# Kernel tuning notes

Measured on AMD Instinct MI355X. Metric: run time of the kernel, lower is better.

The kernel has to match this reference:

```python
import jax, jax.numpy as jnp
import numpy as np

B, N, QD, H, D = 2, 2048, 1152, 16, 72
INNER = H * D
RETAIN_RATE = 0.4  # layer_count in [4, 64] branch
N_KEEP = int(N * RETAIN_RATE)
N_PRUNE = N - N_KEEP
SCALE = D ** (-0.5)


def setup_inputs() -> dict:
    key = jax.random.key(0)
    ks = jax.random.split(key, 6)
    s = 0.02
    return {
        "x": jax.random.normal(ks[0], (B, N, QD), jnp.float32),
        "Wq": jax.random.normal(ks[1], (QD, INNER), jnp.float32) * s,
        "Wk": jax.random.normal(ks[2], (QD, INNER), jnp.float32) * s,
        "Wv": jax.random.normal(ks[3], (QD, INNER), jnp.float32) * s,
        "Wo": jax.random.normal(ks[4], (INNER, QD), jnp.float32) * s,
        "bo": jnp.zeros((QD,), jnp.float32),
    }


def reference(x, Wq, Wk, Wv, Wo, bo):
    b = x.shape[0]
    # self-attention: context = x
    q = (x @ Wq).reshape(b, N, H, D).transpose(0, 2, 1, 3)  # [b,H,N,D]
    k = (x @ Wk).reshape(b, N, H, D).transpose(0, 2, 1, 3)
    v = (x @ Wv).reshape(b, N, H, D).transpose(0, 2, 1, 3)

    # ---- WPR pruning pass: full attention map, mean over heads ----
    logits = jnp.einsum('bhnd,bhmd->bhnm', q, k) * SCALE  # [b,H,N,N]
    M = jax.nn.softmax(logits, axis=-1)
    attn = M.mean(axis=1)  # [b,N,N]

    # 5-step power iteration: dist = (1/N) @ attn^5
    dist = jnp.full((b, 1, N), 1.0 / N, dtype=attn.dtype)
    for _ in range(5):
        dist = dist @ attn
    importance = dist[:, 0]  # [b,N]

    _, imp_inds = jax.lax.top_k(importance, N_KEEP)
    _, prune_inds = jax.lax.top_k(-importance, N_PRUNE)
    # boolean-mask selection in torch returns rows in ascending index order
    sorted_imp = jnp.sort(imp_inds, axis=1)      # [b,N_KEEP]
    sorted_prune = jnp.sort(prune_inds, axis=1)  # [b,N_PRUNE]

    selected_rows = jnp.take_along_axis(attn, sorted_imp[:, :, None], axis=1)  # [b,N_KEEP,N]
    max_inds = jnp.argmax(selected_rows, axis=1)  # [b,N]: most-attending retained row per token
    sim_inds = jnp.take_along_axis(max_inds, sorted_prune, axis=1)  # [b,N_PRUNE]

    # ---- attention among retained tokens only ----
    gi = sorted_imp[:, None, :, None]  # broadcast gather index
    q_r = jnp.take_along_axis(q, gi, axis=2)  # [b,H,N_KEEP,D]
    k_r = jnp.take_along_axis(k, gi, axis=2)
    v_r = jnp.take_along_axis(v, gi, axis=2)
    attn_r = jax.nn.softmax(jnp.einsum('bhnd,bhmd->bhnm', q_r, k_r) * SCALE, axis=-1)
    out_r = jnp.einsum('bhnm,bhmd->bhnd', attn_r, v_r)  # [b,H,N_KEEP,D]
    out_r = out_r.transpose(0, 2, 1, 3).reshape(b, N_KEEP, INNER)

    # similarity-based recovery for pruned tokens
    out_p = jnp.take_along_axis(out_r, sim_inds[:, :, None], axis=1)  # [b,N_PRUNE,INNER]

    bidx = jnp.arange(b)[:, None]
    out = jnp.zeros((b, N, INNER), out_r.dtype)
    out = out.at[bidx, sorted_imp].set(out_r)
    out = out.at[bidx, sorted_prune].set(out_p)

    return out @ Wo + bo
```

## Files before the change

### kernel.cpp

```cpp
#include <hip/hip_runtime.h>

namespace {
constexpr int B = 2;
constexpr int N = 2048;
constexpr int QD = 1152;
constexpr int H = 16;
constexpr int D = 72;
constexpr int INNER = 1152;
constexpr int NKEEP = 819;
constexpr int PSL = 32;
constexpr int ILEN = N / PSL;
constexpr int DP = 80;
constexpr int LSTR = 88;
constexpr int ASL = 16;
constexpr int ACH = (NKEEP + ASL - 1) / ASL;
constexpr int ROWS = B * H * N;
constexpr int X4 = (B * N * QD) / 4;
}

#define FINF __builtin_inff()
#define SCALE 0.11785113019775793f

typedef __attribute__((ext_vector_type(8))) __bf16 bf16x8;
typedef __attribute__((ext_vector_type(16))) float f32x16;
typedef __attribute__((ext_vector_type(8))) short short8;
typedef __attribute__((ext_vector_type(4))) short short4v;

__device__ __forceinline__ f32x16 mfma_bf16(bf16x8 a, bf16x8 b, f32x16 c) {
  return __builtin_amdgcn_mfma_f32_32x32x16_bf16(a, b, c, 0, 0, 0);
}
__device__ __forceinline__ short f2bf(float x) {
  unsigned u = __float_as_uint(x);
  unsigned r = (u + 0x7fffu + ((u >> 16) & 1u)) >> 16;
  return (short)r;
}
__device__ __forceinline__ float bf2f(short b) {
  return __uint_as_float(((unsigned)(unsigned short)b) << 16);
}

__global__ __launch_bounds__(256) void k_prep(
    const float* __restrict__ X, short* __restrict__ Xh, short* __restrict__ Xl,
    short* __restrict__ qkv)
{
  int g = blockIdx.x * 256 + threadIdx.x;
  if (g < X4) {
    float4 v = ((const float4*)X)[g];
    float vv[4] = {v.x, v.y, v.z, v.w};
    short4v h, l;
#pragma unroll
    for (int i = 0; i < 4; ++i) {
      short hb = f2bf(vv[i]);
      h[i] = hb;
      l[i] = f2bf(vv[i] - bf2f(hb));
    }
    *(short4v*)(void*)(Xh + (size_t)g * 4) = h;
    *(short4v*)(void*)(Xl + (size_t)g * 4) = l;
  } else {
    int t = g - X4;
    int arr = t / ROWS, row = t - arr * ROWS;
    *(float4*)(void*)(qkv + (size_t)arr * ROWS * DP + (size_t)row * DP + 72) =
        make_float4(0.f, 0.f, 0.f, 0.f);
  }
}

__global__ __launch_bounds__(256) void k_wsplit4(
    const float* __restrict__ W0, const float* __restrict__ W1,
    const float* __restrict__ W2, const float* __restrict__ W3,
    short* __restrict__ WTh, short* __restrict__ WTl,
    short* __restrict__ WoTh, short* __restrict__ WoTl)
{
  __shared__ float tile[64][65];
  const int tid = threadIdx.x;
  const int k0 = blockIdx.y * 64, n0 = blockIdx.x * 64;
  const int z = blockIdx.z;
  const float* W = (z == 0) ? W0 : (z == 1) ? W1 : (z == 2) ? W2 : W3;
  short* outH = (z < 3) ? WTh + (size_t)z * QD * INNER : WoTh;
  short* outL = (z < 3) ? WTl + (size_t)z * QD * INNER : WoTl;
  {
    int r = tid >> 2, c0 = (tid & 3) * 16;
#pragma unroll
    for (int j = 0; j < 16; j += 4) {
      float4 v = *(const float4*)&W[(size_t)(k0 + r) * 1152 + n0 + c0 + j];
      tile[r][c0 + j] = v.x; tile[r][c0 + j + 1] = v.y;
      tile[r][c0 + j + 2] = v.z; tile[r][c0 + j + 3] = v.w;
    }
  }
  __syncthreads();
  for (int e = tid; e < 4096; e += 256) {
    int nr = e >> 6, kc = e & 63;
    float v = tile[kc][nr];
    short hb = f2bf(v);
    outH[(size_t)(n0 + nr) * 1152 + k0 + kc] = hb;
    outL[(size_t)(n0 + nr) * 1152 + k0 + kc] = f2bf(v - bf2f(hb));
  }
}

__global__ __launch_bounds__(256, 3) void k_pgemm3(
    const short* __restrict__ Ah_g, const short* __restrict__ Al_g,
    const short* __restrict__ Bh_g, const short* __restrict__ Bl_g,
    short* __restrict__ QKV0)
{
  constexpr int LK = 40;
  __shared__ short AhS[128 * LK], AlS[128 * LK], BhS[128 * LK], BlS[128 * LK];
  const int tid = threadIdx.x;
  const int wv = tid >> 6, ln = tid & 63;
  const int col = ln & 31, hi = ln >> 5;
  const int wm = wv >> 1, wn = wv & 1;
  const int swz = (blockIdx.x & 7) * 108 + (blockIdx.x >> 3);
  const int m0 = (swz / 27) * 128, n0 = (swz % 27) * 128;

  f32x16 acc[2][2];
#pragma unroll
  for (int mi = 0; mi < 2; ++mi)
#pragma unroll
    for (int ni = 0; ni < 2; ++ni)
#pragma unroll
      for (int r = 0; r < 16; ++r) acc[mi][ni][r] = 0.f;

  for (int kt = 0; kt < 1152; kt += 32) {
    __syncthreads();
    for (int e = tid; e < 512; e += 256) {
      int r = e >> 2, c4 = e & 3;
      size_t sa = (size_t)(m0 + r) * 1152 + kt + c4 * 8;
      *(float4*)&AhS[r * LK + c4 * 8] = *(const float4*)(Ah_g + sa);
      *(float4*)&AlS[r * LK + c4 * 8] = *(const float4*)(Al_g + sa);
      size_t sb = (size_t)(n0 + r) * 1152 + kt + c4 * 8;
      *(float4*)&BhS[r * LK + c4 * 8] = *(const float4*)(Bh_g + sb);
      *(float4*)&BlS[r * LK + c4 * 8] = *(const float4*)(Bl_g + sb);
    }
    __syncthreads();
#pragma unroll
    for (int kc = 0; kc < 2; ++kc) {
      bf16x8 ah[2], al[2], bh[2], bl[2];
#pragma unroll
      for (int mi = 0; mi < 2; ++mi) {
        int r = wm * 64 + mi * 32 + col;
        ah[mi] = *(const bf16x8*)&AhS[r * LK + kc * 16 + hi * 8];
        al[mi] = *(const bf16x8*)&AlS[r * LK + kc * 16 + hi * 8];
      }
#pragma unroll
      for (int ni = 0; ni < 2; ++ni) {
        int r = wn * 64 + ni * 32 + col;
        bh[ni] = *(const bf16x8*)&BhS[r * LK + kc * 16 + hi * 8];
        bl[ni] = *(const bf16x8*)&BlS[r * LK + kc * 16 + hi * 8];
      }
#pragma unroll
      for (int mi = 0; mi < 2; ++mi)
#pragma unroll
        for (int ni = 0; ni < 2; ++ni) {
          acc[mi][ni] = mfma_bf16(ah[mi], bh[ni], acc[mi][ni]);
          acc[mi][ni] = mfma_bf16(ah[mi], bl[ni], acc[mi][ni]);
          acc[mi][ni] = mfma_bf16(al[mi], bh[ni], acc[mi][ni]);
        }
    }
  }
  const size_t S = (size_t)65536 * 80;
#pragma unroll
  for (int mi = 0; mi < 2; ++mi)
#pragma unroll
    for (int ni = 0; ni < 2; ++ni)
#pragma unroll
      for (int r = 0; r < 16; ++r) {
        int m = m0 + wm * 64 + mi * 32 + (r & 3) + 8 * (r >> 2) + 4 * hi;
        int c = n0 + wn * 64 + ni * 32 + col;
        int which = c / 1152, cm = c - which * 1152;
        int hh = cm / 72, dd = cm - hh * 72;
        int b = m >> 11, nn = m & 2047;
        size_t idx = (((size_t)(b * 16 + hh)) * 2048 + nn) * 80 + dd;
        float v = acc[mi][ni][r];
        short hb = f2bf(v);
        short* OH = QKV0 + (size_t)which * 2 * S;
        OH[idx] = hb;
        OH[S + idx] = f2bf(v - bf2f(hb));
      }
}

__global__ __launch_bounds__(256, 2) void k_stats3(
    const short* __restrict__ Qh, const short* __restrict__ Ql,
    const short* __restrict__ Kh, const short* __restrict__ Kl,
    float* __restrict__ inv_out)
{
  __shared__ __align__(16) short kh[64 * LSTR];
  __shared__ __align__(16) short kl[64 * LSTR];
  const int tid = threadIdx.x;
  const int wv = tid >> 6, ln = tid & 63;
  const int col = ln & 31, hi = ln >> 5;
  const int q0 = blockIdx.x * 256;
  const int h = blockIdx.y, b = blockIdx.z;
  const size_t bhbase = (size_t)(b * H + h) * N * DP;

  bf16x8 qfh[2][5], qfl[2][5];
#pragma unroll
  for (int mi = 0; mi < 2; ++mi) {
    const size_t rb = bhbase + (size_t)(q0 + wv * 64 + mi * 32 + col) * DP + hi * 8;
#pragma unroll
    for (int d = 0; d < 5; ++d) {
      qfh[mi][d] = *(const bf16x8*)(const void*)(Qh + rb + d * 16);
      qfl[mi][d] = *(const bf16x8*)(const void*)(Ql + rb + d * 16);
    }
  }
  float s[2][16];
#pragma unroll
  for (int mi = 0; mi < 2; ++mi)
#pragma unroll
    for (int r = 0; r < 16; ++r) s[mi][r] = 0.f;

  float4 rkh[3], rkl[3];
  auto LOADK = [&](int kt) {
#pragma unroll
    for (int ss = 0; ss < 3; ++ss) {
      int e = ss * 256 + tid;
      if (e < 640) {
        int r = e / 10, cc = e - r * 10;
        size_t sb = bhbase + (size_t)(kt + r) * DP + cc * 8;
        rkh[ss] = *(const float4*)(const void*)(Kh + sb);
        rkl[ss] = *(const float4*)(const void*)(Kl + sb);
      }
    }
  };
  auto STOREK = [&]() {
#pragma unroll
    for (int ss = 0; ss < 3; ++ss) {
      int e = ss * 256 + tid;
      if (e < 640) {
        int r = e / 10, cc = e - r * 10;
        *(float4*)(void*)(kh + r * LSTR + cc * 8) = rkh[ss];
        *(float4*)(void*)(kl + r * LSTR + cc * 8) = rkl[ss];
      }
    }
  };

  LOADK(0);
  for (int kt = 0; kt < N; kt += 64) {
    __syncthreads();
    STOREK();
    __syncthreads();
    if (kt + 64 < N) LOADK(kt + 64);
    f32x16 z[2][2];
#pragma unroll
    for (int mi = 0; mi < 2; ++mi)
#pragma unroll
      for (int rn = 0; rn < 2; ++rn)
#pragma unroll
        for (int r = 0; r < 16; ++r) z[mi][rn][r] = 0.f;
#pragma unroll
    for (int d = 0; d < 5; ++d) {
      const int boff = d * 16 + hi * 8;
      bf16x8 bh0 = *(const bf16x8*)(const void*)(kh + col * LSTR + boff);
      bf16x8 bl0 = *(const bf16x8*)(const void*)(kl + col * LSTR + boff);
      bf16x8 bh1 = *(const bf16x8*)(const void*)(kh + (32 + col) * LSTR + boff);
      bf16x8 bl1 = *(const bf16x8*)(const void*)(kl + (32 + col) * LSTR + boff);
#pragma unroll
      for (int mi = 0; mi < 2; ++mi) {
        z[mi][0] = mfma_bf16(qfh[mi][d], bh0, z[mi][0]);
        z[mi][0] = mfma_bf16(qfh[mi][d], bl0, z[mi][0]);
        z[mi][0] = mfma_bf16(qfl[mi][d], bh0, z[mi][0]);
        z[mi][1] = mfma_bf16(qfh[mi][d], bh1, z[mi][1]);
        z[mi][1] = mfma_bf16(qfh[mi][d], bl1, z[mi][1]);
        z[mi][1] = mfma_bf16(qfl[mi][d], bh1, z[mi][1]);
      }
    }
#pragma unroll
    for (int mi = 0; mi < 2; ++mi)
#pragma unroll
      for (int r = 0; r < 16; ++r)
        s[mi][r] += __expf(z[mi][0][r] * SCALE) + __expf(z[mi][1][r] * SCALE);
  }
#pragma unroll
  for (int mi = 0; mi < 2; ++mi)
#pragma unroll
    for (int r = 0; r < 16; ++r) {
      float v = s[mi][r];
#pragma unroll
      for (int o = 1; o < 32; o <<= 1) v += __shfl_xor(v, o);
      if (col == 0) {
        int row = q0 + wv * 64 + mi * 32 + ((r & 3) + ((r >> 2) << 3) + (hi << 2));
        inv_out[(size_t)(b * H + h) * N + row] = 1.0f / v;
      }
    }
}

__global__ __launch_bounds__(256, 2) void k_attn3(
    const short* __restrict__ Qh, const short* __restrict__ Ql,
    const short* __restrict__ Kh, const short* __restrict__ Kl,
    const float* __restrict__ inv_in, float* __restrict__ attn)
{
  __shared__ __align__(16) short kh[64 * LSTR];
  __shared__ __align__(16) short kl[64 * LSTR];
  __shared__ float invs[256];
  const int tid = threadIdx.x;
  const int wv = tid >> 6, ln = tid & 63;
  const int col = ln & 31, hi = ln >> 5;
  const int k0 = blockIdx.x * 64, q0 = blockIdx.y * 256, b = blockIdx.z;

  f32x16 pa[2][2];
#pragma unroll
  for (int mi = 0; mi < 2; ++mi)
#pragma unroll
    for (int rn = 0; rn < 2; ++rn)
#pragma unroll
      for (int r = 0; r < 16; ++r) pa[mi][rn][r] = 0.f;

  float4 rkh[3], rkl[3];
  float rin;
  auto LOADH = [&](int h) {
    const size_t hb = (size_t)(b * H + h) * N * DP;
#pragma unroll
    for (int ss = 0; ss < 3; ++ss) {
      int e = ss * 256 + tid;
      if (e < 640) {
        int r = e / 10, cc = e - r * 10;
        size_t sb = hb + (size_t)(k0 + r) * DP + cc * 8;
        rkh[ss] = *(const float4*)(const void*)(Kh + sb);
        rkl[ss] = *(const float4*)(const void*)(Kl + sb);
      }
    }
    rin = inv_in[(size_t)(b * H + h) * N + q0 + tid];
  };
  auto STOREH = [&]() {
#pragma unroll
    for (int ss = 0; ss < 3; ++ss) {
      int e = ss * 256 + tid;
      if (e < 640) {
        int r = e / 10, cc = e - r * 10;
        *(float4*)(void*)(kh + r * LSTR + cc * 8) = rkh[ss];
        *(float4*)(void*)(kl + r * LSTR + cc * 8) = rkl[ss];
      }
    }
    invs[tid] = rin;
  };

  LOADH(0);
  for (int h = 0; h < H; ++h) {
    __syncthreads();
    STOREH();
    __syncthreads();
    if (h + 1 < H) LOADH(h + 1);

    const size_t bhbase = (size_t)(b * H + h) * N * DP;
    f32x16 z[2][2];
#pragma unroll
    for (int mi = 0; mi < 2; ++mi)
#pragma unroll
      for (int rn = 0; rn < 2; ++rn)
#pragma unroll
        for (int r = 0; r < 16; ++r) z[mi][rn][r] = 0.f;

#pragma unroll
    for (int d = 0; d < 5; ++d) {
      const int boff = d * 16 + hi * 8;
      bf16x8 bh0 = *(const bf16x8*)(const void*)(kh + col * LSTR + boff);
      bf16x8 bl0 = *(const bf16x8*)(const void*)(kl + col * LSTR + boff);
      bf16x8 bh1 = *(const bf16x8*)(const void*)(kh + (32 + col) * LSTR + boff);
      bf16x8 bl1 = *(const bf16x8*)(const void*)(kl + (32 + col) * LSTR + boff);
      bf16x8 qh0 = *(const bf16x8*)(const void*)(Qh + bhbase + (size_t)(q0 + wv * 64 + col) * DP + boff);
      bf16x8 ql0 = *(const bf16x8*)(const void*)(Ql + bhbase + (size_t)(q0 + wv * 64 + col) * DP + boff);
      bf16x8 qh1 = *(const bf16x8*)(const void*)(Qh + bhbase + (size_t)(q0 + wv * 64 + 32 + col) * DP + boff);
      bf16x8 ql1 = *(const bf16x8*)(const void*)(Ql + bhbase + (size_t)(q0 + wv * 64 + 32 + col) * DP + boff);
      z[0][0] = mfma_bf16(qh0, bh0, z[0][0]);
      z[0][0] = mfma_bf16(qh0, bl0, z[0][0]);
      z[0][0] = mfma_bf16(ql0, bh0, z[0][0]);
      z[0][1] = mfma_bf16(qh0, bh1, z[0][1]);
      z[0][1] = mfma_bf16(qh0, bl1, z[0][1]);
      z[0][1] = mfma_bf16(ql0, bh1, z[0][1]);
      z[1][0] = mfma_bf16(qh1, bh0, z[1][0]);
      z[1][0] = mfma_bf16(qh1, bl0, z[1][0]);
      z[1][0] = mfma_bf16(ql1, bh0, z[1][0]);
      z[1][1] = mfma_bf16(qh1, bh1, z[1][1]);
      z[1][1] = mfma_bf16(qh1, bl1, z[1][1]);
      z[1][1] = mfma_bf16(ql1, bh1, z[1][1]);
    }
#pragma unroll
    for (int mi = 0; mi < 2; ++mi)
#pragma unroll
      for (int r = 0; r < 16; ++r) {
        const int rloc = wv * 64 + mi * 32 + (r & 3) + ((r >> 2) << 3) + (hi << 2);
        const float iv = invs[rloc];
        pa[mi][0][r] += __expf(z[mi][0][r] * SCALE) * iv;
        pa[mi][1][r] += __expf(z[mi][1][r] * SCALE) * iv;
      }
  }
  const float invH = 1.0f / H;
#pragma unroll
  for (int mi = 0; mi < 2; ++mi)
#pragma unroll
    for (int r = 0; r < 16; ++r) {
      const int row = q0 + wv * 64 + mi * 32 + (r & 3) + ((r >> 2) << 3) + (hi << 2);
      attn[((size_t)b * N + row) * N + k0 + col] = pa[mi][0][r] * invH;
      attn[((size_t)b * N + row) * N + k0 + 32 + col] = pa[mi][1][r] * invH;
    }
}

__global__ __launch_bounds__(256) void k_power(
    const float* __restrict__ attn, float* __restrict__ partial)
{
  int g = blockIdx.x * 256 + threadIdx.x;
  int sy = blockIdx.y;
  int b = g / N, j = g % N;
  const float* ab = attn + (size_t)b * N * N;
  int i0 = sy * ILEN;
  float sum = 0.f;
  for (int i = i0; i < i0 + ILEN; ++i) sum += ab[(size_t)i * N + j];
  partial[(size_t)sy * (B * N) + g] = sum * (1.0f / N);
}

__global__ __launch_bounds__(256) void k_powfused(
    const float* __restrict__ attn, const float* __restrict__ partial_in,
    float* __restrict__ partial_out)
{
  __shared__ float red[4][64];
  __shared__ float ds[64];
  const int tid = threadIdx.x;
  const int g = blockIdx.x * 256 + tid;
  const int sy = blockIdx.y;
  const int b = g / N, j = g % N;
  const int i0 = sy * ILEN;
  {
    int i = tid & 63, sgrp = tid >> 6;
    const float* p = partial_in + (size_t)(b * N + i0 + i);
    float s8 = 0.f;
#pragma unroll
    for (int k = 0; k < 8; ++k) s8 += p[(size_t)(sgrp * 8 + k) * (B * N)];
    red[sgrp][i] = s8;
  }
  __syncthreads();
  if (tid < 64) ds[tid] = red[0][tid] + red[1][tid] + red[2][tid] + red[3][tid];
  __syncthreads();
  const float* ab = attn + (size_t)b * N * N;
  float sum = 0.f;
  for (int i = 0; i < ILEN; ++i) sum += ds[i] * ab[(size_t)(i0 + i) * N + j];
  partial_out[(size_t)sy * (B * N) + g] = sum;
}

__global__ __launch_bounds__(1024) void k_partition(
    const float* __restrict__ partial, int* __restrict__ sorted_imp,
    int* __restrict__ keepflag, int* __restrict__ s_map)
{
  __shared__ float v[N];
  __shared__ int   id[N];
  __shared__ int   kf[N];
  __shared__ int   ps[N];
  const int tid = threadIdx.x;
  const int b = blockIdx.x;
  for (int i = tid; i < N; i += 1024) {
    float s = 0.f;
    const float* p = partial + (size_t)(b * N + i);
    for (int sy = 0; sy < PSL; ++sy) s += p[(size_t)sy * (B * N)];
    v[i] = s; id[i] = i;
  }
  for (int k = 2; k <= N; k <<= 1) {
    for (int j = k >> 1; j > 0; j >>= 1) {
      __syncthreads();
      for (int i = tid; i < N; i += 1024) {
        int ixj = i ^ j;
        if (ixj > i) {
          bool up = ((i & k) == 0);
          float va = v[i], vb = v[ixj];
          int ia = id[i], ib = id[ixj];
          bool b_before_a = (vb > va) || (vb == va && ib < ia);
          if (b_before_a == up) { v[i] = vb; v[ixj] = va; id[i] = ib; id[ixj] = ia; }
        }
      }
    }
  }
  __syncthreads();
  for (int i = tid; i < N; i += 1024) kf[id[i]] = (i < NKEEP) ? 1 : 0;
  __syncthreads();
  for (int i = tid; i < N; i += 1024) ps[i] = kf[i];
  for (int off = 1; off < N; off <<= 1) {
    __syncthreads();
    int t0 = (tid >= off) ? ps[tid - off] : 0;
    int i1 = tid + 1024;
    int t1 = ps[i1 - off];
    __syncthreads();
    ps[tid] += t0;
    ps[i1] += t1;
  }
  __syncthreads();
  for (int i = tid; i < N; i += 1024) {
    int excl = ps[i] - kf[i];
    keepflag[b * N + i] = kf[i];
    if (kf[i]) { sorted_imp[b * NKEEP + excl] = i; s_map[b * N + i] = excl; }
  }
}

__global__ __launch_bounds__(256) void k_argmax_part(
    const float* __restrict__ attn, const int* __restrict__ sorted_imp,
    float* __restrict__ pval, int* __restrict__ pidx)
{
  __shared__ int imp_s[ACH];
  const int tid = threadIdx.x;
  const int g = blockIdx.x * 256 + tid;
  const int s = blockIdx.y;
  const int b = g / N, n = g % N;
  const int k0 = s * ACH;
  const int k1 = (k0 + ACH < NKEEP) ? k0 + ACH : NKEEP;
  const int cnt = k1 - k0;
  for (int i = tid; i < cnt; i += 256) imp_s[i] = sorted_imp[b * NKEEP + k0 + i];
  __syncthreads();
  const float* ab = attn + (size_t)b * N * N;
  float best = -FINF; int bi = k0;
  for (int k = 0; k < cnt; ++k) {
    float val = ab[(size_t)imp_s[k] * N + n];
    if (val > best) { best = val; bi = k0 + k; }
  }
  pval[(size_t)s * (B * N) + g] = best;
  pidx[(size_t)s * (B * N) + g] = bi;
}

__global__ __launch_bounds__(256) void k_argmax_comb(
    const float* __restrict__ pval, const int* __restrict__ pidx,
    const int* __restrict__ keepflag, int* __restrict__ s_map)
{
  int g = blockIdx.x * 256 + threadIdx.x;
  if (g >= B * N) return;
  float best = -FINF; int bi = 0;
#pragma unroll
  for (int s = 0; s < ASL; ++s) {
    float v = pval[(size_t)s * (B * N) + g];
    if (v > best) { best = v; bi = pidx[(size_t)s * (B * N) + g]; }
  }
  if (!keepflag[g]) s_map[g] = bi;
}

__global__ __launch_bounds__(256, 2) void k_rfused(
    const short* __restrict__ Qh, const short* __restrict__ Ql,
    const short* __restrict__ Kh, const short* __restrict__ Kl,
    const short* __restrict__ Vh, const int* __restrict__ sorted_imp,
    short* __restrict__ Yh, short* __restrict__ Yl)
{
  constexpr int LK = 88;
  constexpr int VTS = 72;
  __shared__ __align__(16) short KhS[64 * LK];
  __shared__ __align__(16) short KlS[64 * LK];
  __shared__ __align__(16) short VhS[64 * LK];
  __shared__ __align__(16) short VT[72 * VTS];
  __shared__ int imp[NKEEP];
  const int tid = threadIdx.x;
  const int wv = tid >> 6, ln = tid & 63;
  const int col = ln & 31, hi = ln >> 5;
  const int b = blockIdx.z, h = blockIdx.y, q0 = blockIdx.x * 128;
  const size_t bh80 = (size_t)(b * H + h) * N * DP;
  for (int i = tid; i < NKEEP; i += 256) imp[i] = sorted_imp[b * NKEEP + i];
  __syncthreads();
  int qr = q0 + wv * 32 + col;
  int qi = imp[qr < NKEEP ? qr : NKEEP - 1];
  bf16x8 qfh[5], qfl[5];
  {
    const size_t qb = bh80 + (size_t)qi * DP + hi * 8;
#pragma unroll
    for (int d = 0; d < 5; ++d) {
      qfh[d] = *(const bf16x8*)(const void*)(Qh + qb + d * 16);
      qfl[d] = *(const bf16x8*)(const void*)(Ql + qb + d * 16);
    }
  }
  float denom = 0.f;
  f32x16 oacc[3];
#pragma unroll
  for (int nc = 0; nc < 3; ++nc)
#pragma unroll
    for (int r = 0; r < 16; ++r) oacc[nc][r] = 0.f;

  for (int kt = 0; kt < 832; kt += 64) {
    for (int e = tid; e < 640; e += 256) {
      int r = e / 10, cc = e - r * 10;
      int kv = kt + r;
      float4 vkh, vkl, vvh;
      if (kv < NKEEP) {
        size_t sb = bh80 + (size_t)imp[kv] * DP + cc * 8;
        vkh = *(const float4*)(const void*)(Kh + sb);
        vkl = *(const float4*)(const void*)(Kl + sb);
        vvh = *(const float4*)(const void*)(Vh + sb);
      } else {
        vkh = make_float4(0.f, 0.f, 0.f, 0.f); vkl = vkh; vvh = vkh;
      }
      *(float4*)(void*)&KhS[r * LK + cc * 8] = vkh;
      *(float4*)(void*)&KlS[r * LK + cc * 8] = vkl;
      *(float4*)(void*)&VhS[r * LK + cc * 8] = vvh;
    }
    __syncthreads();
    f32x16 z[2];
#pragma unroll
    for (int rn = 0; rn < 2; ++rn)
#pragma unroll
      for (int r = 0; r < 16; ++r) z[rn][r] = 0.f;
#pragma unroll
    for (int d = 0; d < 5; ++d) {
      const int boff = d * 16 + hi * 8;
#pragma unroll
      for (int rn = 0; rn < 2; ++rn) {
        bf16x8 kfh = *(const bf16x8*)(const void*)(KhS + (rn * 32 + col) * LK + boff);
        bf16x8 kfl = *(const bf16x8*)(const void*)(KlS + (rn * 32 + col) * LK + boff);
        z[rn] = mfma_bf16(kfh, qfh[d], z[rn]);
        z[rn] = mfma_bf16(kfh, qfl[d], z[rn]);
        z[rn] = mfma_bf16(kfl, qfh[d], z[rn]);
      }
    }
    for (int e = tid; e < 576; e += 256) {
      int dd = e % 72, k8 = e / 72;
      short8 t;
#pragma unroll
      for (int j = 0; j < 8; ++j) t[j] = VhS[(k8 * 8 + j) * LK + dd];
      *(short8*)(void*)&VT[dd * VTS + k8 * 8] = t;
    }
    const bool full = (kt + 64 <= NKEEP);
#pragma unroll
    for (int rn = 0; rn < 2; ++rn) {
      int kvb = kt + rn * 32 + 4 * hi;
#pragma unroll
      for (int r = 0; r < 16; ++r) {
        float pe = __expf(z[rn][r] * SCALE);
        if (!full) {
          int kv = kvb + (r & 3) + 8 * (r >> 2);
          pe = (kv < NKEEP) ? pe : 0.f;
        }
        z[rn][r] = pe;
        denom += pe;
      }
    }
    __syncthreads();
#pragma unroll
    for (int rn = 0; rn < 2; ++rn) {
#pragma unroll
      for (int kc = 0; kc < 2; ++kc) {
        unsigned p0, p1, p2, p3;
        asm("v_cvt_pk_bf16_f32 %0, %1, %2" : "=v"(p0) : "v"(z[rn][8 * kc + 0]), "v"(z[rn][8 * kc + 1]));
        asm("v_cvt_pk_bf16_f32 %0, %1, %2" : "=v"(p1) : "v"(z[rn][8 * kc + 2]), "v"(z[rn][8 * kc + 3]));
        asm("v_cvt_pk_bf16_f32 %0, %1, %2" : "=v"(p2) : "v"(z[rn][8 * kc + 4]), "v"(z[rn][8 * kc + 5]));
        asm("v_cvt_pk_bf16_f32 %0, %1, %2" : "=v"(p3) : "v"(z[rn][8 * kc + 6]), "v"(z[rn][8 * kc + 7]));
        unsigned othA = hi ? p0 : p2, othB = hi ? p1 : p3;
        unsigned swA = (unsigned)__shfl_xor((int)othA, 32);
        unsigned swB = (unsigned)__shfl_xor((int)othB, 32);
        union { unsigned u[4]; bf16x8 v; } pf;
        pf.u[0] = hi ? swA : p0; pf.u[1] = hi ? swB : p1;
        pf.u[2] = hi ? p2 : swA; pf.u[3] = hi ? p3 : swB;
        const int kb = rn * 32 + kc * 16 + hi * 8;
#pragma unroll
        for (int nc = 0; nc < 3; ++nc) {
          int dr = nc * 32 + col; if (dr > 71) dr = 71;
          bf16x8 vf = *(const bf16x8*)(const void*)(VT + dr * VTS + kb);
          oacc[nc] = mfma_bf16(pf.v, vf, oacc[nc]);
        }
      }
    }
  }
  denom += __shfl_xor(denom, 32);
  float invd = 1.0f / denom;
#pragma unroll
  for (int r = 0; r < 16; ++r) {
    int cr = (r & 3) + 8 * (r >> 2) + 4 * hi;
    int q = q0 + wv * 32 + cr;
    float dv = __shfl(invd, cr);
    if (q < NKEEP) {
#pragma unroll
      for (int nc = 0; nc < 3; ++nc) {
        int dd = nc * 32 + col;
        if (dd < 72) {
          float v = oacc[nc][r] * dv;
          size_t idx = ((size_t)b * NKEEP + q) * 1152 + h * 72 + dd;
          short hb = f2bf(v);
          Yh[idx] = hb;
          Yl[idx] = f2bf(v - bf2f(hb));
        }
      }
    }
  }
}

__global__ __launch_bounds__(256, 2) void k_ogemm(
    const short* __restrict__ Ah_g, const short* __restrict__ Al_g,
    const short* __restrict__ Bh_g, const short* __restrict__ Bl_g,
    float* __restrict__ OutF, const float* __restrict__ bias,
    int Mtot)
{
  constexpr int LK = 40;
  __shared__ short AhS[64 * LK], AlS[64 * LK], BhS[64 * LK], BlS[64 * LK];
  const int tid = threadIdx.x;
  const int wv = tid >> 6, ln = tid & 63;
  const int col = ln & 31, hi = ln >> 5;
  const int wm = wv >> 1, wn = wv & 1;
  const int m0 = blockIdx.y * 64, n0 = blockIdx.x * 64;
  f32x16 acc;
#pragma unroll
  for (int r = 0; r < 16; ++r) acc[r] = 0.f;

  for (int kt = 0; kt < 1152; kt += 32) {
    __syncthreads();
    {
      int e = tid;
      int r = e >> 2, c4 = e & 3;
      int ra = m0 + r; if (ra >= Mtot) ra = Mtot - 1;
      size_t sa = (size_t)ra * 1152 + kt + c4 * 8;
      *(float4*)&AhS[r * LK + c4 * 8] = *(const float4*)(Ah_g + sa);
      *(float4*)&AlS[r * LK + c4 * 8] = *(const float4*)(Al_g + sa);
      size_t sb = (size_t)(n0 + r) * 1152 + kt + c4 * 8;
      *(float4*)&BhS[r * LK + c4 * 8] = *(const float4*)(Bh_g + sb);
      *(float4*)&BlS[r * LK + c4 * 8] = *(const float4*)(Bl_g + sb);
    }
    __syncthreads();
#pragma unroll
    for (int kc = 0; kc < 2; ++kc) {
      int ra = wm * 32 + col;
      int rb = wn * 32 + col;
      bf16x8 ah = *(const bf16x8*)&AhS[ra * LK + kc * 16 + hi * 8];
      bf16x8 al = *(const bf16x8*)&AlS[ra * LK + kc * 16 + hi * 8];
      bf16x8 bh = *(const bf16x8*)&BhS[rb * LK + kc * 16 + hi * 8];
      bf16x8 bl = *(const bf16x8*)&BlS[rb * LK + kc * 16 + hi * 8];
      acc = mfma_bf16(ah, bh, acc);
      acc = mfma_bf16(ah, bl, acc);
      acc = mfma_bf16(al, bh, acc);
    }
  }
#pragma unroll
  for (int r = 0; r < 16; ++r) {
    int m = m0 + wm * 32 + (r & 3) + 8 * (r >> 2) + 4 * hi;
    int c = n0 + wn * 32 + col;
    if (m < Mtot) OutF[(size_t)m * 1152 + c] = acc[r] + bias[c];
  }
}

__global__ __launch_bounds__(256) void k_scatter(
    const float* __restrict__ Y, const int* __restrict__ s_map,
    float* __restrict__ out)
{
  size_t g = (size_t)blockIdx.x * 256 + threadIdx.x;
  if (g >= (size_t)B * N * QD) return;
  int c = (int)(g % QD);
  int n_ = (int)((g / QD) % N);
  int b = (int)(g / ((size_t)N * QD));
  int src = s_map[b * N + n_];
  out[g] = Y[((size_t)b * NKEEP + src) * QD + c];
}

extern "C" void kernel_launch(void* const* d_in, const int* in_sizes, int n_in,
                              void* d_out, int out_size, void* d_ws, size_t ws_size,
                              hipStream_t stream)
{
  const float* x  = (const float*)d_in[0];
  const float* Wq = (const float*)d_in[1];
  const float* Wk = (const float*)d_in[2];
  const float* Wv = (const float*)d_in[3];
  const float* Wo = (const float*)d_in[4];
  const float* bo = (const float*)d_in[5];
  float* out = (float*)d_out;

  char* ws = (char*)d_ws;
  size_t off = 0;
  auto alloc = [&](size_t bytes) -> void* {
    void* p = ws + off;
    off = (off + bytes + 255) & ~(size_t)255;
    return p;
  };
  const size_t XEL = (size_t)B * N * QD;
  const size_t WEL = (size_t)QD * INNER;
  short* xh   = (short*)alloc(sizeof(short) * XEL);
  short* xl   = (short*)alloc(sizeof(short) * XEL);
  short* WTh  = (short*)alloc(sizeof(short) * WEL * 3);
  short* WTl  = (short*)alloc(sizeof(short) * WEL * 3);
  short* WoTh = (short*)alloc(sizeof(short) * WEL);
  short* WoTl = (short*)alloc(sizeof(short) * WEL);
  short* Qhb  = (short*)alloc(sizeof(short) * (size_t)ROWS * DP);
  short* Qlb  = (short*)alloc(sizeof(short) * (size_t)ROWS * DP);
  short* Khb  = (short*)alloc(sizeof(short) * (size_t)ROWS * DP);
  short* Klb  = (short*)alloc(sizeof(short) * (size_t)ROWS * DP);
  short* Vhb  = (short*)alloc(sizeof(short) * (size_t)ROWS * DP);
  short* Vlb  = (short*)alloc(sizeof(short) * (size_t)ROWS * DP);
  float* attn = (float*)alloc(sizeof(float) * (size_t)B * N * N);
  float* inv  = (float*)alloc(sizeof(float) * (size_t)ROWS);
  float* partA = (float*)alloc(sizeof(float) * PSL * B * N);
  float* partB = (float*)alloc(sizeof(float) * PSL * B * N);
  int* sorted_imp = (int*)alloc(sizeof(int) * B * NKEEP);
  int* keepflag   = (int*)alloc(sizeof(int) * B * N);
  int* s_map      = (int*)alloc(sizeof(int) * B * N);
  float* pval     = (float*)alloc(sizeof(float) * ASL * B * N);
  int*   pidx     = (int*)alloc(sizeof(int) * ASL * B * N);
  (void)Vlb;
  short* Yh = xh;
  short* Yl = xh + (size_t)B * NKEEP * INNER;
  float* Y  = (float*)xl;

  dim3 blk(256);

  k_prep<<<dim3((X4 + 6 * ROWS) / 256), blk, 0, stream>>>(x, xh, xl, Qhb);
  k_wsplit4<<<dim3(QD / 64, QD / 64, 4), blk, 0, stream>>>(
      Wq, Wk, Wv, Wo, WTh, WTl, WoTh, WoTl);

  k_pgemm3<<<dim3(864), blk, 0, stream>>>(xh, xl, WTh, WTl, Qhb);

  k_stats3<<<dim3(N / 256, H, B), blk, 0, stream>>>(Qhb, Qlb, Khb, Klb, inv);
  k_attn3<<<dim3(N / 64, N / 256, B), blk, 0, stream>>>(Qhb, Qlb, Khb, Klb, inv, attn);

  k_power<<<dim3(B * N / 256, PSL), blk, 0, stream>>>(attn, partA);
  k_powfused<<<dim3(B * N / 256, PSL), blk, 0, stream>>>(attn, partA, partB);
  k_powfused<<<dim3(B * N / 256, PSL), blk, 0, stream>>>(attn, partB, partA);
  k_powfused<<<dim3(B * N / 256, PSL), blk, 0, stream>>>(attn, partA, partB);
  k_powfused<<<dim3(B * N / 256, PSL), blk, 0, stream>>>(attn, partB, partA);

  k_partition<<<dim3(B), dim3(1024), 0, stream>>>(partA, sorted_imp, keepflag, s_map);
  k_argmax_part<<<dim3(B * N / 256, ASL), blk, 0, stream>>>(attn, sorted_imp, pval, pidx);
  k_argmax_comb<<<dim3(B * N / 256), blk, 0, stream>>>(pval, pidx, keepflag, s_map);

  k_rfused<<<dim3((NKEEP + 127) / 128, H, B), blk, 0, stream>>>(
      Qhb, Qlb, Khb, Klb, Vhb, sorted_imp, Yh, Yl);

  k_ogemm<<<dim3(QD / 64, (B * NKEEP + 63) / 64), blk, 0, stream>>>(
      Yh, Yl, WoTh, WoTl, Y, bo, B * NKEEP);
  k_scatter<<<dim3((int)(((size_t)B * N * QD + 255) / 256)), blk, 0, stream>>>(Y, s_map, out);
}
```

Measured before the change: 543.7 us.

## Load QKV GEMM tiles directly to LDS with swizzled layout

Replaces the register-staged global-to-LDS copies in the split-bf16 QKV projection GEMM with global_load_lds direct-to-LDS 16-byte loads. The padded row layout becomes a compact XOR-style swizzle so the MFMA fragment reads avoid bank conflicts. Launch bounds occupancy drops from 3 to 2 blocks per CU. This is meant to cut VGPR traffic and LDS footprint in the load path. The load is still not double-buffered, so the wait on vmcnt(0) keeps the load stall exposed.

```diff
diff --git a/kernel.cpp b/kernel.cpp
--- a/kernel.cpp
+++ b/kernel.cpp
@@ -37,6 +37,14 @@
 __device__ __forceinline__ float bf2f(short b) {
   return __uint_as_float(((unsigned)(unsigned short)b) << 16);
 }
+__device__ __forceinline__ void gload16(const short* g, short* l) {
+  __builtin_amdgcn_global_load_lds(
+      (const __attribute__((address_space(1))) unsigned*)g,
+      (__attribute__((address_space(3))) unsigned*)l, 16, 0, 0);
+}
+__device__ __forceinline__ int swslot(int r, int c) {
+  return (4 * r + ((c + ((r >> 1) & 3)) & 3)) * 8;
+}
 
 __global__ __launch_bounds__(256) void k_prep(
     const float* __restrict__ X, short* __restrict__ Xh, short* __restrict__ Xl,
@@ -95,13 +103,13 @@
   }
 }
 
-__global__ __launch_bounds__(256, 3) void k_pgemm3(
+__global__ __launch_bounds__(256, 2) void k_pgemm3(
     const short* __restrict__ Ah_g, const short* __restrict__ Al_g,
     const short* __restrict__ Bh_g, const short* __restrict__ Bl_g,
     short* __restrict__ QKV0)
 {
-  constexpr int LK = 40;
-  __shared__ short AhS[128 * LK], AlS[128 * LK], BhS[128 * LK], BlS[128 * LK];
+  __shared__ __align__(16) short AhS[512 * 8], AlS[512 * 8];
+  __shared__ __align__(16) short BhS[512 * 8], BlS[512 * 8];
   const int tid = threadIdx.x;
   const int wv = tid >> 6, ln = tid & 63;
   const int col = ln & 31, hi = ln >> 5;
@@ -119,30 +127,38 @@
 
   for (int kt = 0; kt < 1152; kt += 32) {
     __syncthreads();
-    for (int e = tid; e < 512; e += 256) {
-      int r = e >> 2, c4 = e & 3;
-      size_t sa = (size_t)(m0 + r) * 1152 + kt + c4 * 8;
-      *(float4*)&AhS[r * LK + c4 * 8] = *(const float4*)(Ah_g + sa);
-      *(float4*)&AlS[r * LK + c4 * 8] = *(const float4*)(Al_g + sa);
-      size_t sb = (size_t)(n0 + r) * 1152 + kt + c4 * 8;
-      *(float4*)&BhS[r * LK + c4 * 8] = *(const float4*)(Bh_g + sb);
-      *(float4*)&BlS[r * LK + c4 * 8] = *(const float4*)(Bl_g + sb);
-    }
+#pragma unroll
+    for (int it = 0; it < 2; ++it) {
+      int t = it * 256 + tid;
+      int r = t >> 2;
+      int c = ((t & 3) - ((r >> 1) & 3)) & 3;
+      size_t sa = (size_t)(m0 + r) * 1152 + kt + c * 8;
+      size_t sb = (size_t)(n0 + r) * 1152 + kt + c * 8;
+      int lb = (it * 256 + wv * 64) * 8;
+      gload16(Ah_g + sa, &AhS[lb]);
+      gload16(Al_g + sa, &AlS[lb]);
+      gload16(Bh_g + sb, &BhS[lb]);
+      gload16(Bl_g + sb, &BlS[lb]);
+    }
+    asm volatile("s_waitcnt vmcnt(0)" ::: "memory");
     __syncthreads();
 #pragma unroll
     for (int kc = 0; kc < 2; ++kc) {
+      const int cc = kc * 2 + hi;
       bf16x8 ah[2], al[2], bh[2], bl[2];
 #pragma unroll
       for (int mi = 0; mi < 2; ++mi) {
         int r = wm * 64 + mi * 32 + col;
-        ah[mi] = *(const bf16x8*)&AhS[r * LK + kc * 16 + hi * 8];
-        al[mi] = *(const bf16x8*)&AlS[r * LK + kc * 16 + hi * 8];
+        int s = swslot(r, cc);
+        ah[mi] = *(const bf16x8*)&AhS[s];
+        al[mi] = *(const bf16x8*)&AlS[s];
       }
 #pragma unroll
       for (int ni = 0; ni < 2; ++ni) {
         int r = wn * 64 + ni * 32 + col;
-        bh[ni] = *(const bf16x8*)&BhS[r * LK + kc * 16 + hi * 8];
-        bl[ni] = *(const bf16x8*)&BlS[r * LK + kc * 16 + hi * 8];
+        int s = swslot(r, cc);
+        bh[ni] = *(const bf16x8*)&BhS[s];
+        bl[ni] = *(const bf16x8*)&BlS[s];
       }
 #pragma unroll
       for (int mi = 0; mi < 2; ++mi)
```

After: 546.9 us. No clear change (+0.6%).

## Fuse first power-iteration step into attention-map kernel via column partial sums

Applied to the files above, without the earlier changes.

The attention-map kernel now reduces its per-tile column sums in shared memory and writes 8 row-slice partials, which stand in for the first power-iteration step. The separate k_power pass over the full attention matrix is removed, and k_powfused takes a variable partial count. This drops one full read of the B*N*N attention map and one launch, at the cost of extra shared memory and a reduction tail in k_attn3. The launch bounds of k_pgemm3 also drop from 3 to 2 waves per SIMD, which gives it more registers but lower occupancy.

```diff
diff --git a/kernel.cpp b/kernel.cpp
--- a/kernel.cpp
+++ b/kernel.cpp
@@ -95,7 +95,7 @@
   }
 }
 
-__global__ __launch_bounds__(256, 3) void k_pgemm3(
+__global__ __launch_bounds__(256, 2) void k_pgemm3(
     const short* __restrict__ Ah_g, const short* __restrict__ Al_g,
     const short* __restrict__ Bh_g, const short* __restrict__ Bl_g,
     short* __restrict__ QKV0)
@@ -283,11 +283,13 @@
 __global__ __launch_bounds__(256, 2) void k_attn3(
     const short* __restrict__ Qh, const short* __restrict__ Ql,
     const short* __restrict__ Kh, const short* __restrict__ Kl,
-    const float* __restrict__ inv_in, float* __restrict__ attn)
+    const float* __restrict__ inv_in, float* __restrict__ attn,
+    float* __restrict__ part8)
 {
   __shared__ __align__(16) short kh[64 * LSTR];
   __shared__ __align__(16) short kl[64 * LSTR];
   __shared__ float invs[256];
+  __shared__ float colred[64][8];
   const int tid = threadIdx.x;
   const int wv = tid >> 6, ln = tid & 63;
   const int col = ln & 31, hi = ln >> 5;
@@ -389,24 +391,28 @@
       attn[((size_t)b * N + row) * N + k0 + col] = pa[mi][0][r] * invH;
       attn[((size_t)b * N + row) * N + k0 + 32 + col] = pa[mi][1][r] * invH;
     }
-}
-
-__global__ __launch_bounds__(256) void k_power(
-    const float* __restrict__ attn, float* __restrict__ partial)
-{
-  int g = blockIdx.x * 256 + threadIdx.x;
-  int sy = blockIdx.y;
-  int b = g / N, j = g % N;
-  const float* ab = attn + (size_t)b * N * N;
-  int i0 = sy * ILEN;
-  float sum = 0.f;
-  for (int i = i0; i < i0 + ILEN; ++i) sum += ab[(size_t)i * N + j];
-  partial[(size_t)sy * (B * N) + g] = sum * (1.0f / N);
+  __syncthreads();
+#pragma unroll
+  for (int rn = 0; rn < 2; ++rn) {
+    float s = 0.f;
+#pragma unroll
+    for (int mi = 0; mi < 2; ++mi)
+#pragma unroll
+      for (int r = 0; r < 16; ++r) s += pa[mi][rn][r];
+    colred[rn * 32 + col][wv * 2 + hi] = s * invH;
+  }
+  __syncthreads();
+  if (tid < 64) {
+    float s = 0.f;
+#pragma unroll
+    for (int u = 0; u < 8; ++u) s += colred[tid][u];
+    part8[(size_t)(q0 >> 8) * (B * N) + b * N + k0 + tid] = s * (1.0f / N);
+  }
 }
 
 __global__ __launch_bounds__(256) void k_powfused(
     const float* __restrict__ attn, const float* __restrict__ partial_in,
-    float* __restrict__ partial_out)
+    float* __restrict__ partial_out, int nin)
 {
   __shared__ float red[4][64];
   __shared__ float ds[64];
@@ -417,10 +423,10 @@
   const int i0 = sy * ILEN;
   {
     int i = tid & 63, sgrp = tid >> 6;
+    const int per = nin >> 2;
     const float* p = partial_in + (size_t)(b * N + i0 + i);
     float s8 = 0.f;
-#pragma unroll
-    for (int k = 0; k < 8; ++k) s8 += p[(size_t)(sgrp * 8 + k) * (B * N)];
+    for (int k = 0; k < per; ++k) s8 += p[(size_t)(sgrp * per + k) * (B * N)];
     red[sgrp][i] = s8;
   }
   __syncthreads();
@@ -788,15 +794,15 @@
   k_pgemm3<<<dim3(864), blk, 0, stream>>>(xh, xl, WTh, WTl, Qhb);
 
   k_stats3<<<dim3(N / 256, H, B), blk, 0, stream>>>(Qhb, Qlb, Khb, Klb, inv);
-  k_attn3<<<dim3(N / 64, N / 256, B), blk, 0, stream>>>(Qhb, Qlb, Khb, Klb, inv, attn);
-
-  k_power<<<dim3(B * N / 256, PSL), blk, 0, stream>>>(attn, partA);
-  k_powfused<<<dim3(B * N / 256, PSL), blk, 0, stream>>>(attn, partA, partB);
-  k_powfused<<<dim3(B * N / 256, PSL), blk, 0, stream>>>(attn, partB, partA);
-  k_powfused<<<dim3(B * N / 256, PSL), blk, 0, stream>>>(attn, partA, partB);
-  k_powfused<<<dim3(B * N / 256, PSL), blk, 0, stream>>>(attn, partB, partA);
-
-  k_partition<<<dim3(B), dim3(1024), 0, stream>>>(partA, sorted_imp, keepflag, s_map);
+  k_attn3<<<dim3(N / 64, N / 256, B), blk, 0, stream>>>(
+      Qhb, Qlb, Khb, Klb, inv, attn, partB);
+
+  k_powfused<<<dim3(B * N / 256, PSL), blk, 0, stream>>>(attn, partB, partA, 8);
+  k_powfused<<<dim3(B * N / 256, PSL), blk, 0, stream>>>(attn, partA, partB, 32);
+  k_powfused<<<dim3(B * N / 256, PSL), blk, 0, stream>>>(attn, partB, partA, 32);
+  k_powfused<<<dim3(B * N / 256, PSL), blk, 0, stream>>>(attn, partA, partB, 32);
+
+  k_partition<<<dim3(B), dim3(1024), 0, stream>>>(partB, sorted_imp, keepflag, s_map);
   k_argmax_part<<<dim3(B * N / 256, ASL), blk, 0, stream>>>(attn, sorted_imp, pval, pidx);
   k_argmax_comb<<<dim3(B * N / 256), blk, 0, stream>>>(pval, pidx, keepflag, s_map);
 
```

Result: no change. 540.5 us (-0.6%).
